# Kernel tuning notes

Hardware: AMD Instinct MI355X
Metric: run time of the kernel (lower is better)

Reference implementation:

```python
import jax, jax.numpy as jnp
import numpy as np

B, Q, K, H = 4, 128, 1024, 256
QS, KS, DV = 256, 256, 256


def setup_inputs() -> dict:
    key = jax.random.key(0)
    k1, k2, k3, k4, k5, k6, k7 = jax.random.split(key, 7)
    return {
        "queries": jax.random.normal(k1, (B, Q, QS), dtype=jnp.float32),
        "keys": jax.random.normal(k2, (B, K, KS), dtype=jnp.float32),
        "values": jax.random.normal(k3, (B, K, DV), dtype=jnp.float32),
        "valid_lens": jax.random.randint(k4, (B,), 1, K, dtype=jnp.int64),
        "Wq": jax.random.normal(k5, (QS, H), dtype=jnp.float32) / np.sqrt(QS),
        "Wk": jax.random.normal(k6, (KS, H), dtype=jnp.float32) / np.sqrt(KS),
        "Wv": jax.random.normal(k7, (H,), dtype=jnp.float32) / np.sqrt(H),
    }


def reference(queries, keys, values, valid_lens, Wq, Wk, Wv):
    # Projections: [B,Q,H] and [B,K,H]
    q = jnp.einsum("bqe,eh->bqh", queries, Wq)
    k = jnp.einsum("bke,eh->bkh", keys, Wk)
    # Broadcast add + tanh: [B,Q,K,H] intermediate (the kernel-headroom op)
    feats = jnp.tanh(q[:, :, None, :] + k[:, None, :, :])
    # hidden -> 1 reduction: scores [B,Q,K]
    scores = jnp.einsum("bqkh,h->bqk", feats, Wv)
    # masked softmax: positions >= valid_len set to -1e6 (as in sequence_mask)
    mask = jnp.arange(scores.shape[-1])[None, None, :] < valid_lens[:, None, None]
    scores = jnp.where(mask, scores, jnp.float32(-1e6))
    attn = jax.nn.softmax(scores, axis=-1)
    # dropout is identity in eval mode
    return jnp.einsum("bqk,bkv->bqv", attn, values)
```

## Files before the change

kernel.cpp:

```cpp
#include <hip/hip_runtime.h>

#define NB 4
#define NQ 128
#define NK 1024
#define NH 256
#define NE 256
#define NV 256

#define TSCALE 2.8853900817779268f
#define LOG2E  1.4426950408889634f

static __device__ __forceinline__ float fexp2(float x){ return __builtin_amdgcn_exp2f(x); }
static __device__ __forceinline__ float frcp (float x){ return __builtin_amdgcn_rcpf(x); }
static __device__ __forceinline__ float tanh_of(float x){
    float e = fexp2(x * TSCALE);
    return fmaf(-2.0f, frcp(e + 1.0f), 1.0f);
}

__global__ __launch_bounds__(256) void proj_kernel(
    const float* __restrict__ qin, const float* __restrict__ kin,
    const float* __restrict__ Wq, const float* __restrict__ Wk,
    const float* __restrict__ Wv,
    float4* __restrict__ qdatA, float4* __restrict__ qdatB,
    float4* __restrict__ kTt) {
    const int tid = threadIdx.x;
    const int bi  = blockIdx.x;
    __shared__ float tr[NH][9];
    if (bi < NB * 32) {
        const int row0 = bi * 4;
        const float* r0 = qin + row0 * NE;
        float a0 = 0.f, a1 = 0.f, a2 = 0.f, a3 = 0.f;
#pragma unroll 2
        for (int e = 0; e < NE; e += 4) {
            float4 q0 = *(const float4*)(r0 + e);
            float4 q1 = *(const float4*)(r0 + NE + e);
            float4 q2 = *(const float4*)(r0 + 2 * NE + e);
            float4 q3 = *(const float4*)(r0 + 3 * NE + e);
#pragma unroll
            for (int j = 0; j < 4; ++j) {
                float w = Wq[(e + j) * NH + tid];
                a0 = fmaf(((const float*)&q0)[j], w, a0);
                a1 = fmaf(((const float*)&q1)[j], w, a1);
                a2 = fmaf(((const float*)&q2)[j], w, a2);
                a3 = fmaf(((const float*)&q3)[j], w, a3);
            }
        }
        float wv = Wv[tid];
        float t0 = tanh_of(a0), t1 = tanh_of(a1), t2 = tanh_of(a2), t3 = tanh_of(a3);
        qdatA[bi * NH + tid] = make_float4(t0, wv * t0, t1, wv * t1);
        qdatB[bi * NH + tid] = make_float4(t2, wv * t2, t3, wv * t3);
    } else {
        const int kb = bi - NB * 32;
        const int b  = kb >> 7;
        const int k0 = (kb & 127) * 8;
        const int c   = k0 >> 6;
        const int kl0 = k0 & 63;
        const float* kr = kin + (b * NK + k0) * NE;
        float acc[8] = {0.f,0.f,0.f,0.f,0.f,0.f,0.f,0.f};
#pragma unroll 2
        for (int e = 0; e < NE; e += 4) {
            float4 kvv[8];
#pragma unroll
            for (int i = 0; i < 8; ++i) kvv[i] = *(const float4*)(kr + i * NE + e);
#pragma unroll
            for (int j = 0; j < 4; ++j) {
                float w = Wk[(e + j) * NH + tid];
#pragma unroll
                for (int i = 0; i < 8; ++i)
                    acc[i] = fmaf(((const float*)&kvv[i])[j], w, acc[i]);
            }
        }
#pragma unroll
        for (int i = 0; i < 8; ++i) tr[tid][i] = tanh_of(acc[i]);
        __syncthreads();
#pragma unroll
        for (int p = 0; p < 2; ++p) {
            int idx2 = p * 256 + tid;
            int hg = idx2 >> 3;
            int kk = idx2 & 7;
            float4 v = make_float4(tr[hg*4+0][kk], tr[hg*4+1][kk],
                                   tr[hg*4+2][kk], tr[hg*4+3][kk]);
            kTt[((b * 16 + c) * 64 + hg) * 64 + kl0 + kk] = v;
        }
    }
}

static __device__ __forceinline__ void step4(
    float4 kv4, const float4* __restrict__ qA, const float4* __restrict__ qB,
    const float4* __restrict__ Wv4, int h4,
    float& acc0, float& acc1, float& acc2, float& acc3) {
    float4 wv4 = Wv4[h4];
#pragma unroll
    for (int j = 0; j < 4; ++j) {
        float kv  = (j==0)?kv4.x:(j==1)?kv4.y:(j==2)?kv4.z:kv4.w;
        float wvj = (j==0)?wv4.x:(j==1)?wv4.y:(j==2)?wv4.z:wv4.w;
        float wvb = wvj * kv;
        float4 qa = qA[h4 * 4 + j];
        float4 qb = qB[h4 * 4 + j];
        float p0 = fmaf(qa.x, kv, 1.0f), nu0 = qa.y + wvb;
        float p1 = fmaf(qa.z, kv, 1.0f), nu1 = qa.w + wvb;
        float p2 = fmaf(qb.x, kv, 1.0f), nu2 = qb.y + wvb;
        float p3 = fmaf(qb.z, kv, 1.0f), nu3 = qb.w + wvb;
        float ab = p0 * p1, cd = p2 * p3;
        float r  = frcp(ab * cd);
        float rab = r * cd, rcd = r * ab;
        acc0 = fmaf(nu0, rab * p1, acc0);
        acc1 = fmaf(nu1, rab * p0, acc1);
        acc2 = fmaf(nu2, rcd * p3, acc2);
        acc3 = fmaf(nu3, rcd * p2, acc3);
    }
}

__global__ __launch_bounds__(256) void attn_kernel(
    const float4* __restrict__ qdatA, const float4* __restrict__ qdatB,
    const float4* __restrict__ kTt, const float* __restrict__ V,
    const int* __restrict__ vlen, const float4* __restrict__ Wv4,
    float* __restrict__ part_m, float* __restrict__ part_s,
    float* __restrict__ part_pv) {
    const int tid = threadIdx.x, lane = tid & 63, wvid = tid >> 6;
    const int n0 = (vlen[0] + 63) >> 6, n1 = (vlen[1] + 63) >> 6;
    const int n2 = (vlen[2] + 63) >> 6, n3 = (vlen[3] + 63) >> 6;
    const int G  = n0 + n1 + n2 + n3;
    const int bi = blockIdx.x;
    const int xcd = bi & 7;
    const int jj  = bi >> 3;
    const int qq  = jj & 31;
    const int gs  = ((jj >> 5) << 3) + xcd;
    if (gs >= G) return;
    int b, chunk;
    if      (gs < n0)           { b = 0; chunk = gs; }
    else if (gs < n0 + n1)      { b = 1; chunk = gs - n0; }
    else if (gs < n0 + n1 + n2) { b = 2; chunk = gs - n0 - n1; }
    else                        { b = 3; chunk = gs - n0 - n1 - n2; }
    const int vl    = vlen[b];
    const int k0    = chunk * 64;
    const int k     = k0 + lane;
    const int pidx  = (b * 32 + qq) * 16 + chunk;
    float* pm  = part_m + pidx * 4;
    float* ps  = part_s + pidx * 4;
    float* ppv = part_pv + pidx * (4 * NV);

    __shared__ float red17[4][64 * 17];
    __shared__ float pwS[4][64];

    const float4* qA = qdatA + (b * 32 + qq) * NH;
    const float4* qB = qdatB + (b * 32 + qq) * NH;

    const float4* kp = kTt + ((b * 16 + chunk) * 64 + wvid * 16) * 64 + lane;
    float acc0 = 0.f, acc1 = 0.f, acc2 = 0.f, acc3 = 0.f;
#pragma unroll 4
    for (int i = 0; i < 16; ++i) {
        float4 kv4 = kp[i * 64];
        step4(kv4, qA, qB, Wv4, wvid * 16 + i, acc0, acc1, acc2, acc3);
    }
    {
        float* hp = &red17[wvid][lane * 17];
        hp[0] = acc0; hp[1] = acc1; hp[2] = acc2; hp[3] = acc3;
    }
    __syncthreads();
    {
        const int row = wvid;
        float s = red17[0][lane * 17 + row] + red17[1][lane * 17 + row]
                + red17[2][lane * 17 + row] + red17[3][lane * 17 + row];
        s = (k < vl) ? s : -1e30f;
        float m = s;
#pragma unroll
        for (int d = 32; d >= 1; d >>= 1) m = fmaxf(m, __shfl_xor(m, d, 64));
        float p = fexp2((s - m) * LOG2E);
        float u = p;
#pragma unroll
        for (int d = 32; d >= 1; d >>= 1) u += __shfl_xor(u, d, 64);
        if (lane == 0) { pm[row] = m; ps[row] = u; }
        pwS[row][lane] = p;
    }
    __syncthreads();
    {
        const float* Vb = V + (b * NK + k0) * NV;
        const int v4 = lane * 4;
        float4 o0 = {0,0,0,0}, o1 = {0,0,0,0}, o2 = {0,0,0,0}, o3 = {0,0,0,0};
#pragma unroll 4
        for (int kk = 0; kk < 16; ++kk) {
            const int kkk = wvid * 16 + kk;
            float p0 = pwS[0][kkk], p1 = pwS[1][kkk];
            float p2 = pwS[2][kkk], p3 = pwS[3][kkk];
            float4 vv = *(const float4*)&Vb[kkk * NV + v4];
            o0.x = fmaf(p0, vv.x, o0.x); o0.y = fmaf(p0, vv.y, o0.y);
            o0.z = fmaf(p0, vv.z, o0.z); o0.w = fmaf(p0, vv.w, o0.w);
            o1.x = fmaf(p1, vv.x, o1.x); o1.y = fmaf(p1, vv.y, o1.y);
            o1.z = fmaf(p1, vv.z, o1.z); o1.w = fmaf(p1, vv.w, o1.w);
            o2.x = fmaf(p2, vv.x, o2.x); o2.y = fmaf(p2, vv.y, o2.y);
            o2.z = fmaf(p2, vv.z, o2.z); o2.w = fmaf(p2, vv.w, o2.w);
            o3.x = fmaf(p3, vv.x, o3.x); o3.y = fmaf(p3, vv.y, o3.y);
            o3.z = fmaf(p3, vv.z, o3.z); o3.w = fmaf(p3, vv.w, o3.w);
        }
        float* pd = &red17[wvid][lane * 17];
        *(float4*)(pd + 0)  = o0;
        *(float4*)(pd + 4)  = o1;
        *(float4*)(pd + 8)  = o2;
        *(float4*)(pd + 12) = o3;
    }
    __syncthreads();
    {
        const int row = tid >> 6, vg = tid & 63;
        float4 r = {0,0,0,0};
#pragma unroll
        for (int ww = 0; ww < 4; ++ww) {
            float4 t = *(const float4*)&red17[ww][vg * 17 + row * 4];
            r.x += t.x; r.y += t.y; r.z += t.z; r.w += t.w;
        }
        *(float4*)&ppv[row * NV + vg * 4] = r;
    }
}

__global__ __launch_bounds__(256) void combine_kernel(
    const float* __restrict__ part_m, const float* __restrict__ part_s,
    const float* __restrict__ part_pv, const int* __restrict__ vlen,
    float* __restrict__ out) {
    const int tid = threadIdx.x;
    const int idx = blockIdx.x;
    const int bi  = idx >> 2;
    const int i   = idx & 3;
    const int b   = bi >> 5;
    const int nb  = (vlen[b] + 63) >> 6;
    const int base = bi * 16;
    float M = -1e30f;
    for (int q = 0; q < nb; ++q)
        M = fmaxf(M, part_m[(base + q) * 4 + i]);
    float S = 0.f, o = 0.f;
    for (int q = 0; q < nb; ++q) {
        float wq = fexp2((part_m[(base + q) * 4 + i] - M) * LOG2E);
        S = fmaf(part_s[(base + q) * 4 + i], wq, S);
        o = fmaf(part_pv[((base + q) * 4 + i) * NV + tid], wq, o);
    }
    out[(bi * 4 + i) * NV + tid] = o * frcp(S);
}

extern "C" void kernel_launch(void* const* d_in, const int* in_sizes, int n_in,
                              void* d_out, int out_size, void* d_ws, size_t ws_size,
                              hipStream_t stream) {
    const float* queries = (const float*)d_in[0];
    const float* keys    = (const float*)d_in[1];
    const float* values  = (const float*)d_in[2];
    const int*   vlens   = (const int*)  d_in[3];
    const float* Wq      = (const float*)d_in[4];
    const float* Wk      = (const float*)d_in[5];
    const float* Wv      = (const float*)d_in[6];
    float* out = (float*)d_out;

    float4* qdatA  = (float4*)d_ws;
    float4* qdatB  = qdatA + NB * 32 * NH;
    float4* kTt    = qdatB + NB * 32 * NH;
    float*  part_m = (float*)(kTt + NB * 64 * NK);
    float*  part_s = part_m + 8192;
    float*  part_pv = part_s + 8192;

    proj_kernel   <<<dim3(640), dim3(256), 0, stream>>>(queries, keys, Wq, Wk, Wv,
                                                        qdatA, qdatB, kTt);
    attn_kernel   <<<dim3(2048), dim3(256), 0, stream>>>(qdatA, qdatB, kTt, values,
                                                         vlens, (const float4*)Wv,
                                                         part_m, part_s, part_pv);
    combine_kernel<<<dim3(512), dim3(256), 0, stream>>>(part_m, part_s, part_pv,
                                                        vlens, out);
}
```

Baseline: 125.1 us.

## Process eight query rows per attention block to reuse key and value loads

```diff
diff --git a/kernel.cpp b/kernel.cpp
--- a/kernel.cpp
+++ b/kernel.cpp
@@ -85,32 +85,6 @@
     }
 }
 
-static __device__ __forceinline__ void step4(
-    float4 kv4, const float4* __restrict__ qA, const float4* __restrict__ qB,
-    const float4* __restrict__ Wv4, int h4,
-    float& acc0, float& acc1, float& acc2, float& acc3) {
-    float4 wv4 = Wv4[h4];
-#pragma unroll
-    for (int j = 0; j < 4; ++j) {
-        float kv  = (j==0)?kv4.x:(j==1)?kv4.y:(j==2)?kv4.z:kv4.w;
-        float wvj = (j==0)?wv4.x:(j==1)?wv4.y:(j==2)?wv4.z:wv4.w;
-        float wvb = wvj * kv;
-        float4 qa = qA[h4 * 4 + j];
-        float4 qb = qB[h4 * 4 + j];
-        float p0 = fmaf(qa.x, kv, 1.0f), nu0 = qa.y + wvb;
-        float p1 = fmaf(qa.z, kv, 1.0f), nu1 = qa.w + wvb;
-        float p2 = fmaf(qb.x, kv, 1.0f), nu2 = qb.y + wvb;
-        float p3 = fmaf(qb.z, kv, 1.0f), nu3 = qb.w + wvb;
-        float ab = p0 * p1, cd = p2 * p3;
-        float r  = frcp(ab * cd);
-        float rab = r * cd, rcd = r * ab;
-        acc0 = fmaf(nu0, rab * p1, acc0);
-        acc1 = fmaf(nu1, rab * p0, acc1);
-        acc2 = fmaf(nu2, rcd * p3, acc2);
-        acc3 = fmaf(nu3, rcd * p2, acc3);
-    }
-}
-
 __global__ __launch_bounds__(256) void attn_kernel(
     const float4* __restrict__ qdatA, const float4* __restrict__ qdatB,
     const float4* __restrict__ kTt, const float* __restrict__ V,
@@ -124,8 +98,8 @@
     const int bi = blockIdx.x;
     const int xcd = bi & 7;
     const int jj  = bi >> 3;
-    const int qq  = jj & 31;
-    const int gs  = ((jj >> 5) << 3) + xcd;
+    const int qg  = jj & 15;
+    const int gs  = ((jj >> 4) << 3) + xcd;
     if (gs >= G) return;
     int b, chunk;
     if      (gs < n0)           { b = 0; chunk = gs; }
@@ -135,80 +109,123 @@
     const int vl    = vlen[b];
     const int k0    = chunk * 64;
     const int k     = k0 + lane;
-    const int pidx  = (b * 32 + qq) * 16 + chunk;
-    float* pm  = part_m + pidx * 4;
-    float* ps  = part_s + pidx * 4;
-    float* ppv = part_pv + pidx * (4 * NV);
-
-    __shared__ float red17[4][64 * 17];
-    __shared__ float pwS[4][64];
-
-    const float4* qA = qdatA + (b * 32 + qq) * NH;
-    const float4* qB = qdatB + (b * 32 + qq) * NH;
+    const int pidx  = (b * 16 + qg) * 16 + chunk;
+    float* pm  = part_m + pidx * 8;
+    float* ps  = part_s + pidx * 8;
+    float* ppv = part_pv + pidx * (8 * NV);
+
+    __shared__ float ldsbuf[4][64 * 33];
+    __shared__ float pwS[8][64];
+
+    const int qq0 = qg * 2, qq1 = qg * 2 + 1;
+    const float4* qA0 = qdatA + (b * 32 + qq0) * NH;
+    const float4* qB0 = qdatB + (b * 32 + qq0) * NH;
+    const float4* qA1 = qdatA + (b * 32 + qq1) * NH;
+    const float4* qB1 = qdatB + (b * 32 + qq1) * NH;
 
     const float4* kp = kTt + ((b * 16 + chunk) * 64 + wvid * 16) * 64 + lane;
-    float acc0 = 0.f, acc1 = 0.f, acc2 = 0.f, acc3 = 0.f;
+    float acc[8] = {0.f,0.f,0.f,0.f,0.f,0.f,0.f,0.f};
 #pragma unroll 4
     for (int i = 0; i < 16; ++i) {
         float4 kv4 = kp[i * 64];
-        step4(kv4, qA, qB, Wv4, wvid * 16 + i, acc0, acc1, acc2, acc3);
-    }
-    {
-        float* hp = &red17[wvid][lane * 17];
-        hp[0] = acc0; hp[1] = acc1; hp[2] = acc2; hp[3] = acc3;
+        const int h4 = wvid * 16 + i;
+        float4 wv4 = Wv4[h4];
+#pragma unroll
+        for (int j = 0; j < 4; ++j) {
+            float kv  = (j==0)?kv4.x:(j==1)?kv4.y:(j==2)?kv4.z:kv4.w;
+            float wvj = (j==0)?wv4.x:(j==1)?wv4.y:(j==2)?wv4.z:wv4.w;
+            float wvb = wvj * kv;
+            float4 qa0 = qA0[h4 * 4 + j], qb0 = qB0[h4 * 4 + j];
+            float4 qa1 = qA1[h4 * 4 + j], qb1 = qB1[h4 * 4 + j];
+            float p0 = fmaf(qa0.x, kv, 1.0f), u0 = qa0.y + wvb;
+            float p1 = fmaf(qa0.z, kv, 1.0f), u1 = qa0.w + wvb;
+            float p2 = fmaf(qb0.x, kv, 1.0f), u2 = qb0.y + wvb;
+            float p3 = fmaf(qb0.z, kv, 1.0f), u3 = qb0.w + wvb;
+            float p4 = fmaf(qa1.x, kv, 1.0f), u4 = qa1.y + wvb;
+            float p5 = fmaf(qa1.z, kv, 1.0f), u5 = qa1.w + wvb;
+            float p6 = fmaf(qb1.x, kv, 1.0f), u6 = qb1.y + wvb;
+            float p7 = fmaf(qb1.z, kv, 1.0f), u7 = qb1.w + wvb;
+            float a  = p0 * p1, bb = p2 * p3, c = p4 * p5, d = p6 * p7;
+            float ab = a * bb,  cd = c * d;
+            float r  = frcp(ab * cd);
+            float rab = r * cd, rcd = r * ab;
+            float ia = rab * bb, ib = rab * a;
+            float ic = rcd * d,  id = rcd * c;
+            acc[0] = fmaf(u0, ia * p1, acc[0]);
+            acc[1] = fmaf(u1, ia * p0, acc[1]);
+            acc[2] = fmaf(u2, ib * p3, acc[2]);
+            acc[3] = fmaf(u3, ib * p2, acc[3]);
+            acc[4] = fmaf(u4, ic * p5, acc[4]);
+            acc[5] = fmaf(u5, ic * p4, acc[5]);
+            acc[6] = fmaf(u6, id * p7, acc[6]);
+            acc[7] = fmaf(u7, id * p6, acc[7]);
+        }
+    }
+    {
+        float* hp = &ldsbuf[wvid][lane * 9];
+#pragma unroll
+        for (int r = 0; r < 8; ++r) hp[r] = acc[r];
     }
     __syncthreads();
     {
-        const int row = wvid;
-        float s = red17[0][lane * 17 + row] + red17[1][lane * 17 + row]
-                + red17[2][lane * 17 + row] + red17[3][lane * 17 + row];
-        s = (k < vl) ? s : -1e30f;
-        float m = s;
-#pragma unroll
-        for (int d = 32; d >= 1; d >>= 1) m = fmaxf(m, __shfl_xor(m, d, 64));
-        float p = fexp2((s - m) * LOG2E);
-        float u = p;
-#pragma unroll
-        for (int d = 32; d >= 1; d >>= 1) u += __shfl_xor(u, d, 64);
-        if (lane == 0) { pm[row] = m; ps[row] = u; }
-        pwS[row][lane] = p;
+#pragma unroll
+        for (int rr = 0; rr < 2; ++rr) {
+            const int row = wvid * 2 + rr;
+            float s = ldsbuf[0][lane * 9 + row] + ldsbuf[1][lane * 9 + row]
+                    + ldsbuf[2][lane * 9 + row] + ldsbuf[3][lane * 9 + row];
+            s = (k < vl) ? s : -1e30f;
+            float m = s;
+#pragma unroll
+            for (int d = 32; d >= 1; d >>= 1) m = fmaxf(m, __shfl_xor(m, d, 64));
+            float p = fexp2((s - m) * LOG2E);
+            float u = p;
+#pragma unroll
+            for (int d = 32; d >= 1; d >>= 1) u += __shfl_xor(u, d, 64);
+            if (lane == 0) { pm[row] = m; ps[row] = u; }
+            pwS[row][lane] = p;
+        }
     }
     __syncthreads();
     {
         const float* Vb = V + (b * NK + k0) * NV;
         const int v4 = lane * 4;
-        float4 o0 = {0,0,0,0}, o1 = {0,0,0,0}, o2 = {0,0,0,0}, o3 = {0,0,0,0};
+        float4 o[8];
+#pragma unroll
+        for (int r = 0; r < 8; ++r) o[r] = make_float4(0.f, 0.f, 0.f, 0.f);
 #pragma unroll 4
         for (int kk = 0; kk < 16; ++kk) {
             const int kkk = wvid * 16 + kk;
-            float p0 = pwS[0][kkk], p1 = pwS[1][kkk];
-            float p2 = pwS[2][kkk], p3 = pwS[3][kkk];
             float4 vv = *(const float4*)&Vb[kkk * NV + v4];
-            o0.x = fmaf(p0, vv.x, o0.x); o0.y = fmaf(p0, vv.y, o0.y);
-            o0.z = fmaf(p0, vv.z, o0.z); o0.w = fmaf(p0, vv.w, o0.w);
-            o1.x = fmaf(p1, vv.x, o1.x); o1.y = fmaf(p1, vv.y, o1.y);
-            o1.z = fmaf(p1, vv.z, o1.z); o1.w = fmaf(p1, vv.w, o1.w);
-            o2.x = fmaf(p2, vv.x, o2.x); o2.y = fmaf(p2, vv.y, o2.y);
-            o2.z = fmaf(p2, vv.z, o2.z); o2.w = fmaf(p2, vv.w, o2.w);
-            o3.x = fmaf(p3, vv.x, o3.x); o3.y = fmaf(p3, vv.y, o3.y);
-            o3.z = fmaf(p3, vv.z, o3.z); o3.w = fmaf(p3, vv.w, o3.w);
-        }
-        float* pd = &red17[wvid][lane * 17];
-        *(float4*)(pd + 0)  = o0;
-        *(float4*)(pd + 4)  = o1;
-        *(float4*)(pd + 8)  = o2;
-        *(float4*)(pd + 12) = o3;
+#pragma unroll
+            for (int r = 0; r < 8; ++r) {
+                float p = pwS[r][kkk];
+                o[r].x = fmaf(p, vv.x, o[r].x);
+                o[r].y = fmaf(p, vv.y, o[r].y);
+                o[r].z = fmaf(p, vv.z, o[r].z);
+                o[r].w = fmaf(p, vv.w, o[r].w);
+            }
+        }
+        float* pd = &ldsbuf[wvid][lane * 33];
+#pragma unroll
+        for (int r = 0; r < 8; ++r) {
+            pd[r * 4 + 0] = o[r].x; pd[r * 4 + 1] = o[r].y;
+            pd[r * 4 + 2] = o[r].z; pd[r * 4 + 3] = o[r].w;
+        }
     }
     __syncthreads();
     {
-        const int row = tid >> 6, vg = tid & 63;
-        float4 r = {0,0,0,0};
-#pragma unroll
-        for (int ww = 0; ww < 4; ++ww) {
-            float4 t = *(const float4*)&red17[ww][vg * 17 + row * 4];
-            r.x += t.x; r.y += t.y; r.z += t.z; r.w += t.w;
-        }
-        *(float4*)&ppv[row * NV + vg * 4] = r;
+        const int vg = tid & 63;
+#pragma unroll
+        for (int rr = 0; rr < 2; ++rr) {
+            const int row = rr * 4 + (tid >> 6);
+            float4 r4 = {0,0,0,0};
+#pragma unroll
+            for (int ww = 0; ww < 4; ++ww) {
+                const float* ps2 = &ldsbuf[ww][vg * 33 + row * 4];
+                r4.x += ps2[0]; r4.y += ps2[1]; r4.z += ps2[2]; r4.w += ps2[3];
+            }
+            *(float4*)&ppv[row * NV + vg * 4] = r4;
+        }
     }
 }
 
@@ -218,21 +235,22 @@
     float* __restrict__ out) {
     const int tid = threadIdx.x;
     const int idx = blockIdx.x;
-    const int bi  = idx >> 2;
-    const int i   = idx & 3;
-    const int b   = bi >> 5;
+    const int row = idx & 7;
+    const int qg  = (idx >> 3) & 15;
+    const int b   = idx >> 7;
     const int nb  = (vlen[b] + 63) >> 6;
-    const int base = bi * 16;
+    const int base = (b * 16 + qg) * 16;
     float M = -1e30f;
     for (int q = 0; q < nb; ++q)
-        M = fmaxf(M, part_m[(base + q) * 4 + i]);
+        M = fmaxf(M, part_m[(base + q) * 8 + row]);
     float S = 0.f, o = 0.f;
     for (int q = 0; q < nb; ++q) {
-        float wq = fexp2((part_m[(base + q) * 4 + i] - M) * LOG2E);
-        S = fmaf(part_s[(base + q) * 4 + i], wq, S);
-        o = fmaf(part_pv[((base + q) * 4 + i) * NV + tid], wq, o);
-    }
-    out[(bi * 4 + i) * NV + tid] = o * frcp(S);
+        float wq = fexp2((part_m[(base + q) * 8 + row] - M) * LOG2E);
+        S = fmaf(part_s[(base + q) * 8 + row], wq, S);
+        o = fmaf(part_pv[((base + q) * 8 + row) * NV + tid], wq, o);
+    }
+    const int qq = qg * 2 + (row >> 2);
+    out[((b * 32 + qq) * 4 + (row & 3)) * NV + tid] = o * frcp(S);
 }
 
 extern "C" void kernel_launch(void* const* d_in, const int* in_sizes, int n_in,
@@ -251,12 +269,12 @@
     float4* qdatB  = qdatA + NB * 32 * NH;
     float4* kTt    = qdatB + NB * 32 * NH;
     float*  part_m = (float*)(kTt + NB * 64 * NK);
-    float*  part_s = part_m + 8192;
-    float*  part_pv = part_s + 8192;
+    float*  part_s = part_m + 16384;
+    float*  part_pv = part_s + 16384;
 
     proj_kernel   <<<dim3(640), dim3(256), 0, stream>>>(queries, keys, Wq, Wk, Wv,
                                                         qdatA, qdatB, kTt);
-    attn_kernel   <<<dim3(2048), dim3(256), 0, stream>>>(qdatA, qdatB, kTt, values,
+    attn_kernel   <<<dim3(1024), dim3(256), 0, stream>>>(qdatA, qdatB, kTt, values,
                                                          vlens, (const float4*)Wv,
                                                          part_m, part_s, part_pv);
     combine_kernel<<<dim3(512), dim3(256), 0, stream>>>(part_m, part_s, part_pv,
```

Result: slower. 133.8 us (+6.9%).
